# Performance work log

Measured on AMD Instinct MI355X. Metric: run time of the kernel, lower is better.

## Reference

```python
import jax, jax.numpy as jnp
import numpy as np
from jax import lax

DN = ('NCHW', 'OIHW', 'NCHW')

def conv2d(x, w, b, stride):
    y = lax.conv_general_dilated(x, w, (stride, stride), [(1, 1), (1, 1)], dimension_numbers=DN)
    return y + b[None, :, None, None]

def conv_transpose2d(x, w, b):
    # PyTorch ConvTranspose2d(k=3, stride=2, padding=1, output_padding=1)
    # == conv with lhs_dilation=2, pad low = k-1-p = 1, pad high = k-1-p+op = 2,
    # kernel spatially flipped and in/out channel dims swapped.  w: [in, out, kh, kw]
    wf = jnp.flip(w, (2, 3)).transpose(1, 0, 2, 3)  # [out, in, kh, kw]
    y = lax.conv_general_dilated(x, wf, (1, 1), [(1, 2), (1, 2)], lhs_dilation=(2, 2), dimension_numbers=DN)
    return y + b[None, :, None, None]

def setup_inputs() -> dict:
    key = jax.random.key(0)
    ks = jax.random.split(key, 20)
    s = 0.05
    inp = {
        'x':   jax.random.normal(ks[0], (64, 2, 256, 256), jnp.float32),
        'w1':  jax.random.normal(ks[1], (32, 2, 3, 3), jnp.float32) * s,
        'b1':  jnp.zeros((32,), jnp.float32),
        'w2':  jax.random.normal(ks[2], (64, 32, 3, 3), jnp.float32) * s,
        'b2':  jnp.zeros((64,), jnp.float32),
        'w3':  jax.random.normal(ks[3], (128, 64, 3, 3), jnp.float32) * s,
        'b3':  jnp.zeros((128,), jnp.float32),
        'w4':  jax.random.normal(ks[4], (128, 128, 3, 3), jnp.float32) * s,
        'b4':  jnp.zeros((128,), jnp.float32),
        'emb': jax.random.normal(ks[5], (512, 64), jnp.float32) * s,
        'dw1': jax.random.normal(ks[6], (128, 64, 3, 3), jnp.float32) * s,   # ConvTranspose2d weight [in, out, kh, kw]
        'db1': jnp.zeros((64,), jnp.float32),
        'dw2': jax.random.normal(ks[7], (64, 32, 3, 3), jnp.float32) * s,
        'db2': jnp.zeros((32,), jnp.float32),
        'dw3': jax.random.normal(ks[8], (32, 1, 3, 3), jnp.float32) * s,
        'db3': jnp.zeros((1,), jnp.float32),
    }
    return inp

def reference(x, w1, b1, w2, b2, w3, b3, w4, b4, emb, dw1, db1, dw2, db2, dw3, db3):
    # ---- Encoder ----
    h = jax.nn.relu(conv2d(x, w1, b1, 2))
    h = jax.nn.relu(conv2d(h, w2, b2, 2))
    h = jax.nn.relu(conv2d(h, w3, b3, 2))
    encoded = jax.nn.relu(conv2d(h, w4, b4, 1))  # [B, 128, H/8, W/8]

    # ---- VectorQuantizerEMA (inference math: cdist + argmin + lookup, straight-through) ----
    D = emb.shape[1]  # 64
    flat = encoded.reshape(encoded.shape[0], encoded.shape[1], -1).reshape(-1, D)  # [N, 64]
    dist = (jnp.sum(flat * flat, axis=1, keepdims=True)
            - 2.0 * flat @ emb.T
            + jnp.sum(emb * emb, axis=1)[None, :])  # [N, 512]
    idx = jnp.argmin(dist, axis=1)  # [N]
    quantized = emb[idx]            # [N, 64] gather
    q_st = flat + lax.stop_gradient(quantized - flat)  # straight-through estimator
    vq_feature = q_st.reshape(encoded.shape)

    # ---- Decoder ----
    d = jax.nn.relu(conv_transpose2d(vq_feature, dw1, db1))
    d = jax.nn.relu(conv_transpose2d(d, dw2, db2))
    decoded = conv_transpose2d(d, dw3, db3)  # [B, 1, 256, 256]
    return decoded
```

## Files before the change

### kernel.cpp

```cpp
#include <hip/hip_runtime.h>


using short8  = __attribute__((ext_vector_type(8))) short;
using short4v = __attribute__((ext_vector_type(4))) short;
using floatx4 = __attribute__((ext_vector_type(4))) float;

__device__ inline unsigned short bf16rn(float f) {
  unsigned u = __float_as_uint(f);
  unsigned r = (u + 0x7fffu + ((u >> 16) & 1u)) >> 16;
  return (unsigned short)r;
}
__device__ inline float bf2f1(short h) {
  return __uint_as_float(((unsigned)(unsigned short)h) << 16);
}

__device__ const int DKY[9]  = {1, 1, 1, 2, 0, 2, 2, 0, 0};
__device__ const int DKX[9]  = {1, 2, 0, 1, 1, 2, 0, 2, 0};

__global__ __launch_bounds__(256) void ring_zero(short* __restrict__ h,
                                                 short* __restrict__ l,
                                                 int nimg, int PH, int PW, int C) {
  const int RC = (2 * PW + 2 * (PH - 2)) * C;
  int t = blockIdx.x * 256 + threadIdx.x;
  if (t >= nimg * RC) return;
  const int nl = t / RC;
  int rem = t - nl * RC;
  const int p = rem / C;
  const int ch = rem - p * C;
  int r, c;
  if (p < 2 * PW) {
    r = (p < PW) ? 0 : PH - 1;
    c = (p < PW) ? p : p - PW;
  } else {
    int q = p - 2 * PW;
    if (q < PH - 2) { r = 1 + q; c = 0; }
    else { r = 1 + q - (PH - 2); c = PW - 1; }
  }
  const size_t a = (((size_t)nl * PH + r) * PW + c) * C + ch;
  h[a] = 0; l[a] = 0;
}

__global__ __launch_bounds__(256) void ring_zero1(short* __restrict__ h,
                                                  int nimg, int PH, int PW, int C) {
  const int RC = (2 * PW + 2 * (PH - 2)) * C;
  int t = blockIdx.x * 256 + threadIdx.x;
  if (t >= nimg * RC) return;
  const int nl = t / RC;
  int rem = t - nl * RC;
  const int p = rem / C;
  const int ch = rem - p * C;
  int r, c;
  if (p < 2 * PW) {
    r = (p < PW) ? 0 : PH - 1;
    c = (p < PW) ? p : p - PW;
  } else {
    int q = p - 2 * PW;
    if (q < PH - 2) { r = 1 + q; c = 0; }
    else { r = 1 + q - (PH - 2); c = PW - 1; }
  }
  h[(((size_t)nl * PH + r) * PW + c) * C + ch] = 0;
}

__global__ __launch_bounds__(256) void conv1_xt(const float* __restrict__ x,
                                                const float* __restrict__ w,
                                                const float* __restrict__ bias,
                                                short* __restrict__ oh,
                                                short* __restrict__ ol, int NH) {
  int t = blockIdx.x * 256 + threadIdx.x;
  if (t >= NH * 128 * 128) return;
  const int px = t & 16383;
  const int n  = t >> 14;
  const int r = px >> 7, c = px & 127;
  const int ih0 = 2 * r - 1, iw0 = 2 * c - 1;
  float acc[32];
#pragma unroll
  for (int o = 0; o < 32; ++o) acc[o] = bias[o];
  const float* ip = x + (size_t)n * 2 * 65536;
#pragma unroll
  for (int ic = 0; ic < 2; ++ic, ip += 65536) {
    float v[9];
#pragma unroll
    for (int kh = 0; kh < 3; ++kh) {
      const int ih = ih0 + kh;
#pragma unroll
      for (int kw = 0; kw < 3; ++kw) {
        const int iw = iw0 + kw;
        const bool ok = (ih >= 0) && (ih < 256) && (iw >= 0) && (iw < 256);
        v[kh * 3 + kw] = ok ? ip[ih * 256 + iw] : 0.f;
      }
    }
#pragma unroll
    for (int o = 0; o < 32; ++o) {
      float s = acc[o];
#pragma unroll
      for (int k = 0; k < 9; ++k) s = fmaf(v[k], w[(o * 2 + ic) * 9 + k], s);
      acc[o] = s;
    }
  }
  const size_t base = (((size_t)n * 130 + r + 1) * 130 + (c + 1)) * 32;
  short8 vh[4], vl[4];
#pragma unroll
  for (int g = 0; g < 4; ++g) {
#pragma unroll
    for (int kk = 0; kk < 8; ++kk) {
      const float rv = fmaxf(acc[g * 8 + kk], 0.f);
      const unsigned short hh = bf16rn(rv);
      vh[g][kk] = (short)hh;
      vl[g][kk] = (short)bf16rn(rv - __uint_as_float((unsigned)hh << 16));
    }
    *(short8*)(oh + base + g * 8) = vh[g];
    *(short8*)(ol + base + g * 8) = vl[g];
  }
}

template<int CIN, int COUT>
__global__ __launch_bounds__(256) void wprep_conv(const float* __restrict__ w,
                                                  short* __restrict__ hi,
                                                  short* __restrict__ lo) {
  constexpr int MT = COUT / 16;
  const int t = blockIdx.x * 256 + threadIdx.x;
  const int j = t & 7;
  const int lane = (t >> 3) & 63;
  const int g = t >> 9;
  const int mt = g % MT;
  const int s = g / MT;
  const int icb = s / 9, tap = s - icb * 9;
  const int kh = tap / 3, kw = tap - kh * 3;
  const int m = mt * 16 + (lane & 15);
  const int ic = icb * 32 + ((lane >> 4) << 3) + j;
  const float v = w[((m * CIN + ic) * 3 + kh) * 3 + kw];
  const unsigned short h = bf16rn(v);
  hi[t] = (short)h;
  lo[t] = (short)bf16rn(v - __uint_as_float((unsigned)h << 16));
}

template<int CIN, int COUT>
__global__ __launch_bounds__(256) void wprep_dec_h(const float* __restrict__ w,
                                                   short* __restrict__ hi) {
  constexpr int MT = COUT / 16, ICB = CIN / 32;
  const int t = blockIdx.x * 256 + threadIdx.x;
  const int j = t & 7;
  const int lane = (t >> 3) & 63;
  const int g = t >> 9;
  const int mt = g % MT;
  const int u = g / MT;
  const int icb = u % ICB;
  const int e = u / ICB;
  const int ky = DKY[e], kx = DKX[e];
  const int m = mt * 16 + (lane & 15);
  const int ic = icb * 32 + ((lane >> 4) << 3) + j;
  hi[t] = (short)bf16rn(w[((ic * COUT + m) * 3 + ky) * 3 + kx]);
}

template<int CIN, int COUT, int OH, int OW, int S, int PHI, int PWI, int PHO, int PWO, int NP>
__global__ __launch_bounds__(256) void conv_mfma_xt(
    const short* __restrict__ xih, const short* __restrict__ xil,
    const short* __restrict__ ah,  const short* __restrict__ al,
    const float* __restrict__ bias,
    short* __restrict__ xoh, short* __restrict__ xol) {
  constexpr int MT = COUT / 16, ICB = CIN / 32;
  constexpr int PXB = 64 * NP, TPB = OH * OW / PXB;
  const int b = blockIdx.x;
  const int n = b / TPB, pt = b % TPB;
  const int lane = threadIdx.x & 63, wave = threadIdx.x >> 6;
  const int quad = lane >> 4;
  int rr[NP], cc[NP];
  size_t bbase[NP];
#pragma unroll
  for (int p = 0; p < NP; ++p) {
    const int pl = pt * PXB + wave * (16 * NP) + p * 16 + (lane & 15);
    rr[p] = pl / OW; cc[p] = pl % OW;
    bbase[p] = (((size_t)n * PHI + S * rr[p]) * PWI + S * cc[p]) * CIN + quad * 8;
  }

  floatx4 acc[MT][NP];
#pragma unroll
  for (int mt = 0; mt < MT; ++mt)
#pragma unroll
    for (int p = 0; p < NP; ++p) acc[mt][p] = (floatx4){0.f, 0.f, 0.f, 0.f};

  const short8* __restrict__ ah8 = (const short8*)ah;
  const short8* __restrict__ al8 = (const short8*)al;

  for (int icb = 0; icb < ICB; ++icb) {
#pragma unroll
    for (int tap = 0; tap < 9; ++tap) {
      const int kh = tap / 3, kw = tap - kh * 3;
      short8 bh[NP], bl[NP];
#pragma unroll
      for (int p = 0; p < NP; ++p) {
        const size_t be = bbase[p] + (size_t)(kh * PWI + kw) * CIN + icb * 32;
        bh[p] = *(const short8*)(xih + be);
        bl[p] = *(const short8*)(xil + be);
      }
#pragma unroll
      for (int mt = 0; mt < MT; ++mt) {
        const int fi = ((icb * 9 + tap) * MT + mt) * 64 + lane;
        const short8 wh = ah8[fi];
        const short8 wl = al8[fi];
#pragma unroll
        for (int p = 0; p < NP; ++p) {
          acc[mt][p] = __builtin_amdgcn_mfma_f32_16x16x32_bf16(wh, bh[p], acc[mt][p], 0, 0, 0);
          acc[mt][p] = __builtin_amdgcn_mfma_f32_16x16x32_bf16(wh, bl[p], acc[mt][p], 0, 0, 0);
          acc[mt][p] = __builtin_amdgcn_mfma_f32_16x16x32_bf16(wl, bh[p], acc[mt][p], 0, 0, 0);
        }
      }
    }
  }
#pragma unroll
  for (int p = 0; p < NP; ++p) {
    const size_t ob = (((size_t)n * PHO + rr[p] + 1) * PWO + (cc[p] + 1)) * COUT + quad * 4;
#pragma unroll
    for (int mt = 0; mt < MT; ++mt) {
      short4v sh, sl;
#pragma unroll
      for (int q = 0; q < 4; ++q) {
        const float v = fmaxf(acc[mt][p][q] + bias[mt * 16 + quad * 4 + q], 0.f);
        const unsigned short hh = bf16rn(v);
        sh[q] = (short)hh;
        sl[q] = (short)bf16rn(v - __uint_as_float((unsigned)hh << 16));
      }
      *(short4v*)(xoh + ob + mt * 16) = sh;
      *(short4v*)(xol + ob + mt * 16) = sl;
    }
  }
}

template<int CIN, int COUT, int IH, int IW, int PHI, int PWI, int PHO, int PWO, int NP>
__global__ __launch_bounds__(256) void deconv_bf16_xt(
    const short* __restrict__ xih, const short* __restrict__ ah,
    const float* __restrict__ bias, short* __restrict__ xoh) {
  constexpr int MT = COUT / 16, ICB = CIN / 32;
  constexpr int PXB = 64 * NP, TPB = IH * IW / PXB;
  constexpr int PHE[9] = {0, 1, 1, 2, 2, 3, 3, 3, 3};
  constexpr int DE[9]  = {0, 0, 1, 0, 2, 0, 1, 2, 3};
  const int b = blockIdx.x;
  const int n = b / TPB, pt = b % TPB;
  const int lane = threadIdx.x & 63, wave = threadIdx.x >> 6;
  const int quad = lane >> 4;
  int ii[NP], jj[NP];
  size_t p00[NP];
#pragma unroll
  for (int p = 0; p < NP; ++p) {
    const int pl = pt * PXB + wave * (16 * NP) + p * 16 + (lane & 15);
    ii[p] = pl / IW; jj[p] = pl % IW;
    p00[p] = (((size_t)n * PHI + (ii[p] + 1)) * PWI + (jj[p] + 1)) * CIN + quad * 8;
  }

  floatx4 acc[4][MT][NP];
#pragma unroll
  for (int ph = 0; ph < 4; ++ph)
#pragma unroll
    for (int mt = 0; mt < MT; ++mt)
#pragma unroll
      for (int p = 0; p < NP; ++p) acc[ph][mt][p] = (floatx4){0.f, 0.f, 0.f, 0.f};

  const short8* __restrict__ ah8 = (const short8*)ah;
  for (int icb = 0; icb < ICB; ++icb) {
    short8 bh[NP][4];
#pragma unroll
    for (int p = 0; p < NP; ++p)
#pragma unroll
      for (int d = 0; d < 4; ++d)
        bh[p][d] = *(const short8*)(xih + p00[p] +
                                    (size_t)((d >> 1) * PWI + (d & 1)) * CIN + icb * 32);
#pragma unroll
    for (int e = 0; e < 9; ++e) {
      const int ph = PHE[e], d = DE[e];
#pragma unroll
      for (int mt = 0; mt < MT; ++mt) {
        const short8 wh = ah8[((e * ICB + icb) * MT + mt) * 64 + lane];
#pragma unroll
        for (int p = 0; p < NP; ++p)
          acc[ph][mt][p] = __builtin_amdgcn_mfma_f32_16x16x32_bf16(
              wh, bh[p][d], acc[ph][mt][p], 0, 0, 0);
      }
    }
  }
#pragma unroll
  for (int p = 0; p < NP; ++p)
#pragma unroll
    for (int ph = 0; ph < 4; ++ph) {
      const int oy = 2 * ii[p] + (ph >> 1), ox = 2 * jj[p] + (ph & 1);
      const size_t ob = (((size_t)n * PHO + oy + 1) * PWO + (ox + 1)) * COUT + quad * 4;
#pragma unroll
      for (int mt = 0; mt < MT; ++mt) {
        short4v sh;
#pragma unroll
        for (int q = 0; q < 4; ++q)
          sh[q] = (short)bf16rn(fmaxf(acc[ph][mt][p][q] + bias[mt * 16 + quad * 4 + q], 0.f));
        *(short4v*)(xoh + ob + mt * 16) = sh;
      }
    }
}

__global__ __launch_bounds__(256) void conv4_mfma(
    const short* __restrict__ xthi, const short* __restrict__ xtlo,
    const short* __restrict__ ahi,  const short* __restrict__ alo,
    const float* __restrict__ bias,
    short* __restrict__ ench, short* __restrict__ encl) {
  __shared__ short lh[6 * 34 * 32];
  __shared__ short ll[6 * 34 * 32];
  __shared__ short ash[2][4096];
  __shared__ short asl[2][4096];
  const int b    = blockIdx.x;
  const int n    = b >> 3;
  const int pt   = b & 7;
  const int r0   = pt * 4;
  const int tid  = threadIdx.x;
  const int lane = tid & 63;
  const int wave = tid >> 6;
  const int kq   = lane >> 4;
  int pl[2], lrow[2], lcol[2];
#pragma unroll
  for (int p = 0; p < 2; ++p) {
    pl[p] = pt * 128 + wave * 32 + p * 16 + (lane & 15);
    lrow[p] = (pl[p] >> 5) - r0;
    lcol[p] = pl[p] & 31;
  }

  floatx4 acc[8][2];
#pragma unroll
  for (int mt = 0; mt < 8; ++mt)
#pragma unroll
    for (int p = 0; p < 2; ++p) acc[mt][p] = (floatx4){0.f, 0.f, 0.f, 0.f};

  const short8* __restrict__ ah8 = (const short8*)ahi;
  const short8* __restrict__ al8 = (const short8*)alo;
  const short* __restrict__ ghbase = xthi + (((size_t)n * 34 + r0) * 34) * 128;
  const short* __restrict__ glbase = xtlo + (((size_t)n * 34 + r0) * 34) * 128;

  short8 rah0, rah1, ral0, ral1;
  rah0 = ah8[tid];        rah1 = ah8[tid + 256];
  ral0 = al8[tid];        ral1 = al8[tid + 256];
  *(short8*)(ash[0] + tid * 8) = rah0;
  *(short8*)(ash[0] + (tid + 256) * 8) = rah1;
  *(short8*)(asl[0] + tid * 8) = ral0;
  *(short8*)(asl[0] + (tid + 256) * 8) = ral1;

  int s = 0;
  for (int icb = 0; icb < 4; ++icb) {
    __syncthreads();
    {
      const short* gh = ghbase + icb * 32;
      const short* gl = glbase + icb * 32;
      for (int t = tid; t < 816; t += 256) {
        const int wr  = t * 8;
        const int row = wr / 1088;
        const int rem = wr - row * 1088;
        const int col = rem >> 5;
        const int ch  = rem & 31;
        const size_t g = ((size_t)(row * 34 + col)) * 128 + ch;
        *(short8*)(lh + wr) = *(const short8*)(gh + g);
        *(short8*)(ll + wr) = *(const short8*)(gl + g);
      }
    }
    __syncthreads();
#pragma unroll
    for (int tap = 0; tap < 9; ++tap, ++s) {
      if (s < 35) {
        const int nb = (s + 1) * 512;
        rah0 = ah8[nb + tid];        rah1 = ah8[nb + tid + 256];
        ral0 = al8[nb + tid];        ral1 = al8[nb + tid + 256];
      }
      const int kh = tap / 3, kw = tap - kh * 3;
      const short8* __restrict__ a8h = (const short8*)ash[s & 1];
      const short8* __restrict__ a8l = (const short8*)asl[s & 1];
      short8 bh[2], bl[2];
#pragma unroll
      for (int p = 0; p < 2; ++p) {
        const int le = ((lrow[p] + kh) * 34 + (lcol[p] + kw)) * 32 + kq * 8;
        bh[p] = *(const short8*)(lh + le);
        bl[p] = *(const short8*)(ll + le);
      }
#pragma unroll
      for (int mt = 0; mt < 8; ++mt) {
        const short8 ah = a8h[mt * 64 + lane];
        const short8 al = a8l[mt * 64 + lane];
#pragma unroll
        for (int p = 0; p < 2; ++p) {
          acc[mt][p] = __builtin_amdgcn_mfma_f32_16x16x32_bf16(ah, bh[p], acc[mt][p], 0, 0, 0);
          acc[mt][p] = __builtin_amdgcn_mfma_f32_16x16x32_bf16(ah, bl[p], acc[mt][p], 0, 0, 0);
          acc[mt][p] = __builtin_amdgcn_mfma_f32_16x16x32_bf16(al, bh[p], acc[mt][p], 0, 0, 0);
        }
      }
      if (s < 35) {
        const int nbuf = (s + 1) & 1;
        *(short8*)(ash[nbuf] + tid * 8) = rah0;
        *(short8*)(ash[nbuf] + (tid + 256) * 8) = rah1;
        *(short8*)(asl[nbuf] + tid * 8) = ral0;
        *(short8*)(asl[nbuf] + (tid + 256) * 8) = ral1;
        __syncthreads();
      }
    }
  }
#pragma unroll
  for (int p = 0; p < 2; ++p) {
    const size_t obase = (size_t)n * 128 * 1024 + pl[p];
#pragma unroll
    for (int mt = 0; mt < 8; ++mt) {
#pragma unroll
      for (int q = 0; q < 4; ++q) {
        const int cout = mt * 16 + kq * 4 + q;
        const float rr = fmaxf(acc[mt][p][q] + bias[cout], 0.f);
        const unsigned short h = bf16rn(rr);
        const size_t oi = obase + (size_t)cout * 1024;
        ench[oi] = (short)h;
        encl[oi] = (short)bf16rn(rr - __uint_as_float((unsigned)h << 16));
      }
    }
  }
}

__global__ __launch_bounds__(256) void vq_norms(const float* __restrict__ emb,
                                                float* __restrict__ norms) {
  int jj = blockIdx.x * 256 + threadIdx.x;
  if (jj < 512) {
    float s = 0.f;
    const float* e = emb + jj * 64;
#pragma unroll
    for (int k = 0; k < 64; ++k) s = fmaf(e[k], e[k], s);
    norms[jj] = s;
  }
}

__global__ __launch_bounds__(256) void emb_prep(const float* __restrict__ emb,
                                                short* __restrict__ hi,
                                                short* __restrict__ lo) {
  const int t = blockIdx.x * 256 + threadIdx.x;
  const int j  = t & 7;
  const int l  = (t >> 3) & 63;
  const int kk = (t >> 9) & 1;
  const int ct = t >> 10;
  const int code = ct * 16 + (l & 15);
  const int k = kk * 32 + ((l >> 4) << 3) + j;
  const float v = emb[code * 64 + k];
  const unsigned short h = bf16rn(v);
  hi[t] = (short)h;
  lo[t] = (short)bf16rn(v - __uint_as_float((unsigned)h << 16));
}

__global__ __launch_bounds__(256) void vq_mfma(
    const short* __restrict__ fhi, const short* __restrict__ flo,
    const short* __restrict__ ebh, const short* __restrict__ ebl,
    const float* __restrict__ nrm, const float* __restrict__ emb,
    short* __restrict__ d1h) {
  __shared__ int sidx[64];
  const int lane = threadIdx.x & 63;
  const int wave = threadIdx.x >> 6;
  const int r0 = blockIdx.x * 64 + wave * 16;
  const size_t abase = ((size_t)(r0 + (lane & 15))) * 64 + ((lane >> 4) << 3);
  short8 ah0 = *(const short8*)(fhi + abase);
  short8 ah1 = *(const short8*)(fhi + abase + 32);
  short8 al0 = *(const short8*)(flo + abase);
  short8 al1 = *(const short8*)(flo + abase + 32);

  float bestv[4] = {3.4e38f, 3.4e38f, 3.4e38f, 3.4e38f};
  int   besti[4] = {0, 0, 0, 0};
  const short8* __restrict__ ebh8 = (const short8*)ebh;
  const short8* __restrict__ ebl8 = (const short8*)ebl;
  for (int ct = 0; ct < 32; ++ct) {
    const int f0 = (ct * 2) * 64 + lane;
    const short8 b0h = ebh8[f0];
    const short8 b1h = ebh8[f0 + 64];
    const short8 b0l = ebl8[f0];
    const short8 b1l = ebl8[f0 + 64];
    floatx4 acc = {0.f, 0.f, 0.f, 0.f};
    acc = __builtin_amdgcn_mfma_f32_16x16x32_bf16(ah0, b0h, acc, 0, 0, 0);
    acc = __builtin_amdgcn_mfma_f32_16x16x32_bf16(ah1, b1h, acc, 0, 0, 0);
    acc = __builtin_amdgcn_mfma_f32_16x16x32_bf16(ah0, b0l, acc, 0, 0, 0);
    acc = __builtin_amdgcn_mfma_f32_16x16x32_bf16(ah1, b1l, acc, 0, 0, 0);
    acc = __builtin_amdgcn_mfma_f32_16x16x32_bf16(al0, b0h, acc, 0, 0, 0);
    acc = __builtin_amdgcn_mfma_f32_16x16x32_bf16(al1, b1h, acc, 0, 0, 0);
    const int code = ct * 16 + (lane & 15);
    const float nn = nrm[code];
#pragma unroll
    for (int q = 0; q < 4; ++q) {
      const float sc = nn - 2.f * acc[q];
      if (sc < bestv[q]) { bestv[q] = sc; besti[q] = code; }
    }
  }
#pragma unroll
  for (int off = 1; off < 16; off <<= 1) {
#pragma unroll
    for (int q = 0; q < 4; ++q) {
      const float ov = __shfl_xor(bestv[q], off, 64);
      const int   oi = __shfl_xor(besti[q], off, 64);
      if (ov < bestv[q] || (ov == bestv[q] && oi < besti[q])) {
        bestv[q] = ov; besti[q] = oi;
      }
    }
  }
  if ((lane & 15) == 0) {
#pragma unroll
    for (int q = 0; q < 4; ++q)
      sidx[wave * 16 + (lane >> 4) * 4 + q] = besti[q];
  }
  __syncthreads();
  const int row  = threadIdx.x >> 2;
  const int part = threadIdx.x & 3;
  const int rid = blockIdx.x * 64 + row;
  const int n  = rid >> 11;
  const int ch = (rid >> 4) & 127;
  const int pb = rid & 15;
  const int gi = sidx[row];
  const float4* src = (const float4*)(emb + (size_t)gi * 64 + part * 16);
  float4 v0 = src[0], v1 = src[1], v2 = src[2], v3 = src[3];
  float vals[16] = {v0.x, v0.y, v0.z, v0.w, v1.x, v1.y, v1.z, v1.w,
                    v2.x, v2.y, v2.z, v2.w, v3.x, v3.y, v3.z, v3.w};
#pragma unroll
  for (int kk = 0; kk < 16; ++kk) {
    const int k = part * 16 + kk;
    const int pix = pb * 64 + k;
    const int r = pix >> 5, c = pix & 31;
    const size_t a = (((size_t)n * 34 + r + 1) * 34 + (c + 1)) * 128 + ch;
    d1h[a] = (short)bf16rn(vals[kk]);
  }
}

__global__ __launch_bounds__(256) void dec3_xt(const short* __restrict__ xh,
                                               const float* __restrict__ w,
                                               const float* __restrict__ bias,
                                               float* __restrict__ out, int NH) {
  int t = blockIdx.x * 256 + threadIdx.x;
  if (t >= NH * 128 * 128) return;
  const int px = t & 16383;
  const int nl = t >> 14;
  const int i = px >> 7, j = px & 127;
  const float b0 = bias[0];
  float a00 = b0, a01 = b0, a10 = b0, a11 = b0;
  const size_t base00 = (((size_t)nl * 130 + i + 1) * 130 + (j + 1)) * 32;
#pragma unroll
  for (int icg = 0; icg < 4; ++icg) {
    const short8 h00 = *(const short8*)(xh + base00 + icg * 8);
    const short8 h01 = *(const short8*)(xh + base00 + 32 + icg * 8);
    const short8 h10 = *(const short8*)(xh + base00 + 130 * 32 + icg * 8);
    const short8 h11 = *(const short8*)(xh + base00 + 130 * 32 + 32 + icg * 8);
#pragma unroll
    for (int kk = 0; kk < 8; ++kk) {
      const int ic = icg * 8 + kk;
      const float x00 = bf2f1(h00[kk]);
      const float x01 = bf2f1(h01[kk]);
      const float x10 = bf2f1(h10[kk]);
      const float x11 = bf2f1(h11[kk]);
      const float* wp = w + ic * 9;
      a00 = fmaf(x00, wp[4], a00);
      a01 = fmaf(x00, wp[5], fmaf(x01, wp[3], a01));
      a10 = fmaf(x00, wp[7], fmaf(x10, wp[1], a10));
      a11 = fmaf(x00, wp[8], fmaf(x01, wp[6], fmaf(x10, wp[2], fmaf(x11, wp[0], a11))));
    }
  }
  float* op = out + ((size_t)nl * 256 + 2 * i) * 256 + 2 * j;
  op[0] = a00; op[1] = a01; op[256] = a10; op[257] = a11;
}

extern "C" void kernel_launch(void* const* d_in, const int* in_sizes, int n_in,
                              void* d_out, int out_size, void* d_ws, size_t ws_size,
                              hipStream_t stream) {
  const float* x   = (const float*)d_in[0];
  const float* w1  = (const float*)d_in[1];
  const float* b1  = (const float*)d_in[2];
  const float* w2  = (const float*)d_in[3];
  const float* b2  = (const float*)d_in[4];
  const float* w3  = (const float*)d_in[5];
  const float* b3  = (const float*)d_in[6];
  const float* w4  = (const float*)d_in[7];
  const float* b4  = (const float*)d_in[8];
  const float* emb = (const float*)d_in[9];
  const float* dw1 = (const float*)d_in[10];
  const float* db1 = (const float*)d_in[11];
  const float* dw2 = (const float*)d_in[12];
  const float* db2 = (const float*)d_in[13];
  const float* dw3 = (const float*)d_in[14];
  const float* db3 = (const float*)d_in[15];
  float* outp = (float*)d_out;

  const int N = in_sizes[0] / (2 * 256 * 256);
  if (N & 1) return;
  const int NH = N / 2;

  const size_t sx3 = (size_t)N * 66 * 66 * 64;
  const size_t sx2 = (size_t)NH * 130 * 130 * 32;
  const size_t sx4 = (size_t)N * 34 * 34 * 128;
  const size_t se  = (size_t)N * 128 * 1024;
  const size_t sd1 = sx4;
  const size_t smalls = 512 + 18432 + 73728 + 147456 + 73728 + 18432 + 32768;
  const size_t need = (sx3 + sx4 + se + sd1 + smalls) * sizeof(float);
  if (ws_size < need) return;

  float* ws = (float*)d_ws;
  short* x3h = (short*)ws;                 short* x3l = x3h + sx3;
  short* x2h = (short*)(ws + sx3);         short* x2l = x2h + sx2;
  short* x4h = (short*)(ws + sx3);         short* x4l = x4h + sx4;
  short* ech = (short*)(ws + sx3 + sx4);   short* ecl = ech + se;
  short* d1h = (short*)(ws + sx3 + sx4 + se);
  short* d2h = (short*)ws;
  short* d3h = (short*)(ws + sx3);
  float* sm  = ws + sx3 + sx4 + se + sd1;
  float* nrm = sm;
  short* a2h = (short*)(sm + 512);                         short* a2l = a2h + 18432;
  short* a3h = (short*)(sm + 512 + 18432);                 short* a3l = a3h + 73728;
  short* a4h = (short*)(sm + 512 + 18432 + 73728);         short* a4l = a4h + 147456;
  short* ad1h = (short*)(sm + 512 + 18432 + 73728 + 147456);
  short* ad2h = (short*)(sm + 512 + 18432 + 73728 + 147456 + 73728);
  short* ebh = (short*)(sm + 512 + 18432 + 73728 + 147456 + 73728 + 18432); short* ebl = ebh + 32768;

  wprep_conv<32, 64><<<72, 256, 0, stream>>>(w2, a2h, a2l);
  wprep_conv<64, 128><<<288, 256, 0, stream>>>(w3, a3h, a3l);
  wprep_conv<128, 128><<<576, 256, 0, stream>>>(w4, a4h, a4l);
  wprep_dec_h<128, 64><<<288, 256, 0, stream>>>(dw1, ad1h);
  wprep_dec_h<64, 32><<<72, 256, 0, stream>>>(dw2, ad2h);
  vq_norms<<<2, 256, 0, stream>>>(emb, nrm);
  emb_prep<<<128, 256, 0, stream>>>(emb, ebh, ebl);

  ring_zero<<<(int)((NH * 516 * 32 + 255) / 256), 256, 0, stream>>>(x2h, x2l, NH, 130, 130, 32);
  ring_zero<<<(int)(((size_t)N * 260 * 64 + 255) / 256), 256, 0, stream>>>(x3h, x3l, N, 66, 66, 64);
  for (int half = 0; half < 2; ++half) {
    const int n0 = half * NH;
    conv1_xt<<<NH * 16384 / 256, 256, 0, stream>>>(
        x + (size_t)n0 * 2 * 65536, w1, b1, x2h, x2l, NH);
    conv_mfma_xt<32, 64, 64, 64, 2, 130, 130, 66, 66, 2>
        <<<NH * 32, 256, 0, stream>>>(x2h, x2l, a2h, a2l, b2,
                                      x3h + (size_t)n0 * 66 * 66 * 64,
                                      x3l + (size_t)n0 * 66 * 66 * 64);
  }
  ring_zero<<<(int)(((size_t)N * 132 * 128 + 255) / 256), 256, 0, stream>>>(x4h, x4l, N, 34, 34, 128);
  conv_mfma_xt<64, 128, 32, 32, 2, 66, 66, 34, 34, 2>
      <<<N * 8, 256, 0, stream>>>(x3h, x3l, a3h, a3l, b3, x4h, x4l);
  conv4_mfma<<<N * 8, 256, 0, stream>>>(x4h, x4l, a4h, a4l, b4, ech, ecl);

  ring_zero1<<<(int)(((size_t)N * 132 * 128 + 255) / 256), 256, 0, stream>>>(d1h, N, 34, 34, 128);
  vq_mfma<<<N * 2048 / 64, 256, 0, stream>>>(ech, ecl, ebh, ebl, nrm, emb, d1h);

  ring_zero1<<<(int)(((size_t)N * 260 * 64 + 255) / 256), 256, 0, stream>>>(d2h, N, 66, 66, 64);
  deconv_bf16_xt<128, 64, 32, 32, 34, 34, 66, 66, 2>
      <<<N * 8, 256, 0, stream>>>(d1h, ad1h, db1, d2h);
  ring_zero1<<<(int)((NH * 516 * 32 + 255) / 256), 256, 0, stream>>>(d3h, NH, 130, 130, 32);
  for (int half = 0; half < 2; ++half) {
    const int n0 = half * NH;
    deconv_bf16_xt<64, 32, 64, 64, 66, 66, 130, 130, 2>
        <<<NH * 32, 256, 0, stream>>>(d2h + (size_t)n0 * 66 * 66 * 64,
                                      ad2h, db2, d3h);
    dec3_xt<<<NH * 16384 / 256, 256, 0, stream>>>(
        d3h, dw3, db3, outp + (size_t)n0 * 65536, NH);
  }
}
```

Baseline: 624.0 us.

## Remap VQ blocks to all channels of a pixel block for vectorized NHWC writes

Each VQ block now covers all 128 channels of one 64-pixel block of one image, so there are half as many blocks and each wave runs two MFMA row groups per codebook tile, reusing the codebook loads. The output scatter into the padded NHWC decoder input changes from scalar 2-byte stores spread across channels to 16-byte short8 stores of 8 contiguous channels. The cost is more registers for the doubled A fragments and accumulators, and scattered gathers from emb, since each lane reads 8 different codebook rows at the same column.

```diff
diff --git a/kernel.cpp b/kernel.cpp
--- a/kernel.cpp
+++ b/kernel.cpp
@@ -445,18 +445,30 @@
     const short* __restrict__ ebh, const short* __restrict__ ebl,
     const float* __restrict__ nrm, const float* __restrict__ emb,
     short* __restrict__ d1h) {
-  __shared__ int sidx[64];
+  __shared__ int sidx[128];
   const int lane = threadIdx.x & 63;
   const int wave = threadIdx.x >> 6;
-  const int r0 = blockIdx.x * 64 + wave * 16;
-  const size_t abase = ((size_t)(r0 + (lane & 15))) * 64 + ((lane >> 4) << 3);
-  short8 ah0 = *(const short8*)(fhi + abase);
-  short8 ah1 = *(const short8*)(fhi + abase + 32);
-  short8 al0 = *(const short8*)(flo + abase);
-  short8 al1 = *(const short8*)(flo + abase + 32);
-
-  float bestv[4] = {3.4e38f, 3.4e38f, 3.4e38f, 3.4e38f};
-  int   besti[4] = {0, 0, 0, 0};
+  const int n  = blockIdx.x >> 4;
+  const int pb = blockIdx.x & 15;
+
+  short8 ah0[2], ah1[2], al0[2], al1[2];
+#pragma unroll
+  for (int g = 0; g < 2; ++g) {
+    const int ch = wave * 32 + g * 16 + (lane & 15);
+    const size_t abase = (((size_t)(n * 128 + ch)) * 16 + pb) * 64 + ((lane >> 4) << 3);
+    ah0[g] = *(const short8*)(fhi + abase);
+    ah1[g] = *(const short8*)(fhi + abase + 32);
+    al0[g] = *(const short8*)(flo + abase);
+    al1[g] = *(const short8*)(flo + abase + 32);
+  }
+
+  float bestv[2][4];
+  int   besti[2][4];
+#pragma unroll
+  for (int g = 0; g < 2; ++g)
+#pragma unroll
+    for (int q = 0; q < 4; ++q) { bestv[g][q] = 3.4e38f; besti[g][q] = 0; }
+
   const short8* __restrict__ ebh8 = (const short8*)ebh;
   const short8* __restrict__ ebl8 = (const short8*)ebl;
   for (int ct = 0; ct < 32; ++ct) {
@@ -465,56 +477,59 @@
     const short8 b1h = ebh8[f0 + 64];
     const short8 b0l = ebl8[f0];
     const short8 b1l = ebl8[f0 + 64];
-    floatx4 acc = {0.f, 0.f, 0.f, 0.f};
-    acc = __builtin_amdgcn_mfma_f32_16x16x32_bf16(ah0, b0h, acc, 0, 0, 0);
-    acc = __builtin_amdgcn_mfma_f32_16x16x32_bf16(ah1, b1h, acc, 0, 0, 0);
-    acc = __builtin_amdgcn_mfma_f32_16x16x32_bf16(ah0, b0l, acc, 0, 0, 0);
-    acc = __builtin_amdgcn_mfma_f32_16x16x32_bf16(ah1, b1l, acc, 0, 0, 0);
-    acc = __builtin_amdgcn_mfma_f32_16x16x32_bf16(al0, b0h, acc, 0, 0, 0);
-    acc = __builtin_amdgcn_mfma_f32_16x16x32_bf16(al1, b1h, acc, 0, 0, 0);
     const int code = ct * 16 + (lane & 15);
     const float nn = nrm[code];
 #pragma unroll
-    for (int q = 0; q < 4; ++q) {
-      const float sc = nn - 2.f * acc[q];
-      if (sc < bestv[q]) { bestv[q] = sc; besti[q] = code; }
+    for (int g = 0; g < 2; ++g) {
+      floatx4 acc = {0.f, 0.f, 0.f, 0.f};
+      acc = __builtin_amdgcn_mfma_f32_16x16x32_bf16(ah0[g], b0h, acc, 0, 0, 0);
+      acc = __builtin_amdgcn_mfma_f32_16x16x32_bf16(ah1[g], b1h, acc, 0, 0, 0);
+      acc = __builtin_amdgcn_mfma_f32_16x16x32_bf16(ah0[g], b0l, acc, 0, 0, 0);
+      acc = __builtin_amdgcn_mfma_f32_16x16x32_bf16(ah1[g], b1l, acc, 0, 0, 0);
+      acc = __builtin_amdgcn_mfma_f32_16x16x32_bf16(al0[g], b0h, acc, 0, 0, 0);
+      acc = __builtin_amdgcn_mfma_f32_16x16x32_bf16(al1[g], b1h, acc, 0, 0, 0);
+#pragma unroll
+      for (int q = 0; q < 4; ++q) {
+        const float sc = nn - 2.f * acc[q];
+        if (sc < bestv[g][q]) { bestv[g][q] = sc; besti[g][q] = code; }
+      }
     }
   }
 #pragma unroll
   for (int off = 1; off < 16; off <<= 1) {
 #pragma unroll
-    for (int q = 0; q < 4; ++q) {
-      const float ov = __shfl_xor(bestv[q], off, 64);
-      const int   oi = __shfl_xor(besti[q], off, 64);
-      if (ov < bestv[q] || (ov == bestv[q] && oi < besti[q])) {
-        bestv[q] = ov; besti[q] = oi;
-      }
-    }
+    for (int g = 0; g < 2; ++g)
+#pragma unroll
+      for (int q = 0; q < 4; ++q) {
+        const float ov = __shfl_xor(bestv[g][q], off, 64);
+        const int   oi = __shfl_xor(besti[g][q], off, 64);
+        if (ov < bestv[g][q] || (ov == bestv[g][q] && oi < besti[g][q])) {
+          bestv[g][q] = ov; besti[g][q] = oi;
+        }
+      }
   }
   if ((lane & 15) == 0) {
 #pragma unroll
-    for (int q = 0; q < 4; ++q)
-      sidx[wave * 16 + (lane >> 4) * 4 + q] = besti[q];
+    for (int g = 0; g < 2; ++g)
+#pragma unroll
+      for (int q = 0; q < 4; ++q)
+        sidx[wave * 32 + g * 16 + (lane >> 4) * 4 + q] = besti[g][q];
   }
   __syncthreads();
-  const int row  = threadIdx.x >> 2;
-  const int part = threadIdx.x & 3;
-  const int rid = blockIdx.x * 64 + row;
-  const int n  = rid >> 11;
-  const int ch = (rid >> 4) & 127;
-  const int pb = rid & 15;
-  const int gi = sidx[row];
-  const float4* src = (const float4*)(emb + (size_t)gi * 64 + part * 16);
-  float4 v0 = src[0], v1 = src[1], v2 = src[2], v3 = src[3];
-  float vals[16] = {v0.x, v0.y, v0.z, v0.w, v1.x, v1.y, v1.z, v1.w,
-                    v2.x, v2.y, v2.z, v2.w, v3.x, v3.y, v3.z, v3.w};
-#pragma unroll
-  for (int kk = 0; kk < 16; ++kk) {
-    const int k = part * 16 + kk;
-    const int pix = pb * 64 + k;
+  const int chg = (threadIdx.x & 15) * 8;
+  int gi8[8];
+#pragma unroll
+  for (int k = 0; k < 8; ++k) gi8[k] = sidx[chg + k];
+#pragma unroll
+  for (int pxg = 0; pxg < 4; ++pxg) {
+    const int p = pxg * 16 + (threadIdx.x >> 4);
+    const int pix = pb * 64 + p;
     const int r = pix >> 5, c = pix & 31;
-    const size_t a = (((size_t)n * 34 + r + 1) * 34 + (c + 1)) * 128 + ch;
-    d1h[a] = (short)bf16rn(vals[kk]);
+    short8 v;
+#pragma unroll
+    for (int k = 0; k < 8; ++k)
+      v[k] = (short)bf16rn(emb[(size_t)gi8[k] * 64 + p]);
+    *(short8*)(d1h + (((size_t)n * 34 + r + 1) * 34 + (c + 1)) * 128 + chg) = v;
   }
 }
 
@@ -630,7 +645,7 @@
   conv4_mfma<<<N * 8, 256, 0, stream>>>(x4h, x4l, a4h, a4l, b4, ech, ecl);
 
   ring_zero1<<<(int)(((size_t)N * 132 * 128 + 255) / 256), 256, 0, stream>>>(d1h, N, 34, 34, 128);
-  vq_mfma<<<N * 2048 / 64, 256, 0, stream>>>(ech, ecl, ebh, ebl, nrm, emb, d1h);
+  vq_mfma<<<N * 16, 256, 0, stream>>>(ech, ecl, ebh, ebl, nrm, emb, d1h);
 
   ring_zero1<<<(int)(((size_t)N * 260 * 64 + 255) / 256), 256, 0, stream>>>(d2h, N, 66, 66, 64);
   deconv_bf16_xt<128, 64, 32, 32, 34, 34, 66, 66, 2>
```

After: 655.8 us. +5.1%, slower.
